# Kernel tuning notes

Hardware: AMD Instinct MI355X
Metric: run time of the kernel (lower is better)

The kernel has to match this reference:

```python
import jax, jax.numpy as jnp
import numpy as np


def quantize_uniform(x, n_bits, clip):
    # clamp to [-clip, clip], round to 2^(1-n_bits)*clip grid, cap at clip*(1-b)
    b = 2.0 ** (1 - n_bits)
    xc = jnp.clip(x, -clip, clip)
    return clip * jnp.minimum(b * jnp.round(xc / (b * clip)), 1.0 - b)


def quantize_act(x, n_bits, clip):
    # clip to [0, clip], round to 2^-n_bits grid, cap at 1 - 2^-n_bits
    s = 2.0 ** n_bits
    xc = jnp.clip(x, 0.0, clip)
    return jnp.minimum(jnp.round(xc * s) / s, 1.0 - 1.0 / s)


def qconv(x, w, b, pad):
    # fake-quantized conv: weights/bias quant(8,1), input quant(8,4), output quant(8,8)
    wq = quantize_uniform(w, 8, 1.0)
    bq = quantize_uniform(b, 8, 1.0)
    xq = quantize_uniform(x, 8, 4.0)
    y = jax.lax.conv_general_dilated(
        xq, wq, window_strides=(1, 1), padding=[(pad, pad), (pad, pad)],
        dimension_numbers=('NCHW', 'OIHW', 'NCHW'))
    y = y + bq[None, :, None, None]
    return quantize_uniform(y, 8, 8.0)


def setup_inputs() -> dict:
    key = jax.random.key(0)
    ks = jax.random.split(key, 7)
    N, Cin, H, W = 32, 128, 56, 56
    Sq, E1, E3 = 32, 128, 128
    x = jax.random.normal(ks[0], (N, Cin, H, W), dtype=jnp.float32)
    w_sq = jax.random.normal(ks[1], (Sq, Cin, 1, 1), dtype=jnp.float32) * 0.05
    b_sq = jax.random.normal(ks[2], (Sq,), dtype=jnp.float32) * 0.05
    w_e1 = jax.random.normal(ks[3], (E1, Sq, 1, 1), dtype=jnp.float32) * 0.05
    b_e1 = jax.random.normal(ks[4], (E1,), dtype=jnp.float32) * 0.05
    w_e3 = jax.random.normal(ks[5], (E3, Sq, 3, 3), dtype=jnp.float32) * 0.05
    b_e3 = jax.random.normal(ks[6], (E3,), dtype=jnp.float32) * 0.05
    return {'x': x, 'w_sq': w_sq, 'b_sq': b_sq, 'w_e1': w_e1, 'b_e1': b_e1,
            'w_e3': w_e3, 'b_e3': b_e3}


def reference(x, w_sq, b_sq, w_e1, b_e1, w_e3, b_e3):
    h = jax.nn.relu(qconv(x, w_sq, b_sq, pad=0))
    h = quantize_act(h, 13, 4.0)
    y1 = jax.nn.relu(qconv(h, w_e1, b_e1, pad=0))
    y3 = jax.nn.relu(qconv(h, w_e3, b_e3, pad=1))
    return jnp.concatenate([y1, y3], axis=1)
```

## Files before the change

### kernel.cpp

```cpp
#include <hip/hip_runtime.h>
#include <stdint.h>

typedef __bf16 bf16x8 __attribute__((ext_vector_type(8)));
typedef float  f32x4  __attribute__((ext_vector_type(4)));

#define HW   3136
#define WID  56
#define CIN  128
#define SQ   32

#define OFF_BSQ 0
#define OFF_BE  32
#define WSQF_BYTES_OFF 1152
#define WE1F_BYTES_OFF 9344
#define WE3F_BYTES_OFF 17536

__device__ __forceinline__ float quant_w8(float x){
  float xc = fminf(fmaxf(x,-1.f),1.f);
  return fminf(rintf(xc*128.f)*0.0078125f, 0.9921875f);
}
__device__ __forceinline__ ushort wq_int_bf16(float x){
  float xc = fminf(fmaxf(x,-1.f),1.f);
  float n = fminf(rintf(xc*128.f), 127.f);
  return (ushort)(__float_as_uint(n)>>16);
}
__device__ __forceinline__ uint pack2f(float a, float b){
  return (__float_as_uint(a)>>16) | (__float_as_uint(b)&0xffff0000u);
}

__global__ void prep_kernel(const float* __restrict__ wsq, const float* __restrict__ bsq,
                            const float* __restrict__ we1, const float* __restrict__ be1,
                            const float* __restrict__ we3, const float* __restrict__ be3,
                            float* __restrict__ ws){
  int tid = blockIdx.x*blockDim.x+threadIdx.x;
  int nth = gridDim.x*blockDim.x;
  ushort* wsqf = (ushort*)((char*)ws + WSQF_BYTES_OFF);
  ushort* we1f = (ushort*)((char*)ws + WE1F_BYTES_OFF);
  ushort* we3f = (ushort*)((char*)ws + WE3F_BYTES_OFF);
  for (int i=tid;i<SQ;i+=nth) ws[OFF_BSQ+i]=quant_w8(bsq[i]);
  for (int i=tid;i<256;i+=nth) ws[OFF_BE+i] = (i<128)? quant_w8(be1[i]) : quant_w8(be3[i-128]);
  for (int i=tid;i<4096;i+=nth){
    int mfkc=i>>9, l=(i>>3)&63, j=i&7;
    int mf=mfkc>>2, kc=mfkc&3;
    int co=mf*16+(l&15), ci=kc*32+(l>>4)*8+j;
    wsqf[i] = wq_int_bf16(wsq[co*CIN+ci]);
  }
  for (int i=tid;i<4096;i+=nth){
    int mf=i>>9, l=(i>>3)&63, j=i&7;
    int co=mf*16+(l&15), ci=(l>>4)*8+j;
    we1f[i] = wq_int_bf16(we1[co*SQ+ci]);
  }
  for (int i=tid;i<36864;i+=nth){
    int mf=i/4608, r=i-mf*4608, t=r>>9, l=(r>>3)&63, j=r&7;
    int co=mf*16+(l&15), ci=(l>>4)*8+j;
    we3f[i] = wq_int_bf16(we3[(co*SQ+ci)*9+t]);
  }
}

__global__ __launch_bounds__(512, 2) void fire_kernel(const float* __restrict__ x,
    const float* __restrict__ ws, float* __restrict__ out){
  __shared__ uint4 lds4[2320];
  int wg = blockIdx.x;
  int logical = (wg & 7)*28 + (wg >> 3);
  int n   = logical/7;
  int bry = logical - n*7;
  int tid = threadIdx.x, w = tid>>6, lane = tid&63;
  int colg = lane&15, kg = lane>>4;
  int R0 = bry*8;
  int vr0 = (R0==0) ? 0 : R0-1;
  int vr1 = (R0+8 > 55) ? 55 : R0+8;
  int limit = (vr1+1)*WID;
  int nblk = ((vr1-vr0+1)*WID + 15)>>4;
  int base_px = vr0*WID;

  uint4 z = make_uint4(0,0,0,0);
  for (int i=tid; i<2320; i+=512) lds4[i] = z;
  __syncthreads();

  {
    const bf16x8* wsqf = (const bf16x8*)((const char*)ws + WSQF_BYTES_OFF);
    bf16x8 W[8];
    #pragma unroll
    for (int q=0;q<8;++q) W[q] = wsqf[q*64 + lane];
    float bias[2][4];
    #pragma unroll
    for (int mf=0;mf<2;++mf)
      #pragma unroll
      for (int r=0;r<4;++r) bias[mf][r] = ws[OFF_BSQ + mf*16 + kg*4 + r];

    for (int b=w; b<nblk; b+=8){
      int px = base_px + b*16 + colg;
      int pxc = (px < limit) ? px : (limit-1);
      const float* xp = x + (size_t)n*CIN*HW + pxc;
      float xv[32];
      #pragma unroll
      for (int kc=0;kc<4;++kc)
        #pragma unroll
        for (int j=0;j<8;++j)
          xv[kc*8+j] = xp[(size_t)(kc*32 + kg*8 + j)*HW];

      bf16x8 Bf[4];
      #pragma unroll
      for (int kc=0;kc<4;++kc){
        float m[8];
        #pragma unroll
        for (int j=0;j<8;++j){
          float v = fminf(fmaxf(xv[kc*8+j],-4.f),4.f);
          m[j] = fminf(rintf(v*32.f), 127.f);
        }
        union { uint u[4]; bf16x8 v; } cv;
        #pragma unroll
        for (int q=0;q<4;++q) cv.u[q] = pack2f(m[q*2], m[q*2+1]);
        Bf[kc] = cv.v;
      }

      f32x4 acc0 = (f32x4){0.f,0.f,0.f,0.f};
      f32x4 acc1 = (f32x4){0.f,0.f,0.f,0.f};
      #pragma unroll
      for (int kc=0;kc<4;++kc){
        acc0 = __builtin_amdgcn_mfma_f32_16x16x32_bf16(W[kc],   Bf[kc], acc0, 0,0,0);
        acc1 = __builtin_amdgcn_mfma_f32_16x16x32_bf16(W[4+kc], Bf[kc], acc1, 0,0,0);
      }

      if (px < limit){
        int rr = px/WID, c = px - rr*WID;
        int ph = (rr - R0 + 1)*58 + c + 1;
        #pragma unroll
        for (int mf=0;mf<2;++mf){
          f32x4 a = mf ? acc1 : acc0;
          float m[4];
          #pragma unroll
          for (int r=0;r<4;++r){
            float y = fmaf(a[r], 0.000244140625f, bias[mf][r]);
            y = fminf(fmaxf(y,-8.f),8.f);
            y = fminf(rintf(y*16.f)*0.0625f, 7.9375f);
            y = fmaxf(y,0.f);
            y = fminf(y,4.f);
            y = fminf(y,0.9998779296875f);
            m[r] = rintf(y*32.f);
          }
          int chunk = mf*2 + (kg>>1);
          int idx = ph*4 + (chunk ^ ((ph>>1)&3));
          uint* dst = (uint*)&lds4[idx] + (kg&1)*2;
          dst[0] = pack2f(m[0], m[1]);
          dst[1] = pack2f(m[2], m[3]);
        }
      }
    }
  }
  __syncthreads();

  int wid = w&3, rpl = w>>2;
  const bf16x8* we1f = (const bf16x8*)((const char*)ws + WE1F_BYTES_OFF);
  const bf16x8* we3f = (const bf16x8*)((const char*)ws + WE3F_BYTES_OFF);
  const bf16x8* lbase = (const bf16x8*)lds4;

  #pragma unroll
  for (int s=0; s<2; ++s){
    int rp = rpl*2 + s;
    int baseh[7];
    #pragma unroll
    for (int nf=0;nf<7;++nf){
      int p = rp*112 + nf*16 + colg;
      int rr = p/WID, c = p - rr*WID;
      baseh[nf] = (rr+1)*58 + c + 1;
    }

    f32x4 acc[4][7];
    #pragma unroll
    for (int mi=0;mi<4;++mi)
      #pragma unroll
      for (int nf=0;nf<7;++nf)
        acc[mi][nf] = (f32x4){0.f,0.f,0.f,0.f};

    #pragma unroll
    for (int t=0;t<9;++t){
      int off = (t/3 - 1)*58 + (t%3 - 1);
      bf16x8 B[7];
      #pragma unroll
      for (int nf=0;nf<7;++nf){
        int ph = baseh[nf] + off;
        int idx = ph*4 + (kg ^ ((ph>>1)&3));
        B[nf] = lbase[idx];
      }
      bf16x8 A2 = we3f[(wid*9+t)*64 + lane];
      bf16x8 A3 = we3f[((wid+4)*9+t)*64 + lane];
      #pragma unroll
      for (int nf=0;nf<7;++nf){
        acc[2][nf] = __builtin_amdgcn_mfma_f32_16x16x32_bf16(B[nf], A2, acc[2][nf], 0,0,0);
        acc[3][nf] = __builtin_amdgcn_mfma_f32_16x16x32_bf16(B[nf], A3, acc[3][nf], 0,0,0);
      }
      if (t==4){
        bf16x8 A0 = we1f[wid*64 + lane];
        bf16x8 A1 = we1f[(wid+4)*64 + lane];
        #pragma unroll
        for (int nf=0;nf<7;++nf){
          acc[0][nf] = __builtin_amdgcn_mfma_f32_16x16x32_bf16(B[nf], A0, acc[0][nf], 0,0,0);
          acc[1][nf] = __builtin_amdgcn_mfma_f32_16x16x32_bf16(B[nf], A1, acc[1][nf], 0,0,0);
        }
      }
    }

    #pragma unroll
    for (int mi=0;mi<4;++mi){
      int co = (wid+mi*4)*16 + colg;
      float bias = ws[OFF_BE + co];
      float* opb = out + (size_t)(n*256+co)*HW + R0*WID + rp*112 + kg*4;
      #pragma unroll
      for (int nf=0;nf<7;++nf){
        f32x4 a = acc[mi][nf];
        f32x4 yv;
        #pragma unroll
        for (int r=0;r<4;++r){
          float y = fmaf(a[r], 0.000244140625f, bias);
          y = fminf(fmaxf(y,-8.f),8.f);
          y = fminf(rintf(y*16.f)*0.0625f, 7.9375f);
          y = fmaxf(y,0.f);
          yv[r] = y;
        }
        *(f32x4*)(opb + nf*16) = yv;
      }
    }
  }
}

extern "C" void kernel_launch(void* const* d_in, const int* in_sizes, int n_in,
                              void* d_out, int out_size, void* d_ws, size_t ws_size,
                              hipStream_t stream){
  const float* x   = (const float*)d_in[0];
  const float* wsq = (const float*)d_in[1];
  const float* bsq = (const float*)d_in[2];
  const float* we1 = (const float*)d_in[3];
  const float* be1 = (const float*)d_in[4];
  const float* we3 = (const float*)d_in[5];
  const float* be3 = (const float*)d_in[6];
  float* out = (float*)d_out;
  float* ws  = (float*)d_ws;

  hipLaunchKernelGGL(prep_kernel, dim3(64), dim3(256), 0, stream,
                     wsq, bsq, we1, be1, we3, be3, ws);
  hipLaunchKernelGGL(fire_kernel, dim3(224), dim3(512), 0, stream, x, ws, out);
}
```

Measured before the change: 43.40 us.

## Fuse weight prep into main kernel and stage quantized weights in LDS

Drops the separate prep kernel launch. Each workgroup now quantizes the squeeze, expand1x1 and expand3x3 weights itself, writes them into shared memory in MFMA fragment layout, and reads the expand weights from LDS instead of global memory. Biases are quantized inline. This removes a launch and the dependency between kernels. In exchange every block repeats the weight quantization with strided global reads, and the extra ~88KB of LDS probably limits occupancy to one block per CU. The epilogue is rewritten with a different channel mapping and leaves a dead loop behind.

Result: slower. 52.72 us (+21.5%).

```diff
diff --git a/kernel.cpp b/kernel.cpp
--- a/kernel.cpp
+++ b/kernel.cpp
@@ -9,57 +9,28 @@
 #define CIN  128
 #define SQ   32
 
-#define OFF_BSQ 0
-#define OFF_BE  32
-#define WSQF_BYTES_OFF 1152
-#define WE1F_BYTES_OFF 9344
-#define WE3F_BYTES_OFF 17536
-
 __device__ __forceinline__ float quant_w8(float x){
   float xc = fminf(fmaxf(x,-1.f),1.f);
   return fminf(rintf(xc*128.f)*0.0078125f, 0.9921875f);
 }
-__device__ __forceinline__ ushort wq_int_bf16(float x){
+__device__ __forceinline__ float wq_int_f(float x){
   float xc = fminf(fmaxf(x,-1.f),1.f);
-  float n = fminf(rintf(xc*128.f), 127.f);
-  return (ushort)(__float_as_uint(n)>>16);
+  return fminf(rintf(xc*128.f), 127.f);
 }
 __device__ __forceinline__ uint pack2f(float a, float b){
   return (__float_as_uint(a)>>16) | (__float_as_uint(b)&0xffff0000u);
 }
 
-__global__ void prep_kernel(const float* __restrict__ wsq, const float* __restrict__ bsq,
-                            const float* __restrict__ we1, const float* __restrict__ be1,
-                            const float* __restrict__ we3, const float* __restrict__ be3,
-                            float* __restrict__ ws){
-  int tid = blockIdx.x*blockDim.x+threadIdx.x;
-  int nth = gridDim.x*blockDim.x;
-  ushort* wsqf = (ushort*)((char*)ws + WSQF_BYTES_OFF);
-  ushort* we1f = (ushort*)((char*)ws + WE1F_BYTES_OFF);
-  ushort* we3f = (ushort*)((char*)ws + WE3F_BYTES_OFF);
-  for (int i=tid;i<SQ;i+=nth) ws[OFF_BSQ+i]=quant_w8(bsq[i]);
-  for (int i=tid;i<256;i+=nth) ws[OFF_BE+i] = (i<128)? quant_w8(be1[i]) : quant_w8(be3[i-128]);
-  for (int i=tid;i<4096;i+=nth){
-    int mfkc=i>>9, l=(i>>3)&63, j=i&7;
-    int mf=mfkc>>2, kc=mfkc&3;
-    int co=mf*16+(l&15), ci=kc*32+(l>>4)*8+j;
-    wsqf[i] = wq_int_bf16(wsq[co*CIN+ci]);
-  }
-  for (int i=tid;i<4096;i+=nth){
-    int mf=i>>9, l=(i>>3)&63, j=i&7;
-    int co=mf*16+(l&15), ci=(l>>4)*8+j;
-    we1f[i] = wq_int_bf16(we1[co*SQ+ci]);
-  }
-  for (int i=tid;i<36864;i+=nth){
-    int mf=i/4608, r=i-mf*4608, t=r>>9, l=(r>>3)&63, j=r&7;
-    int co=mf*16+(l&15), ci=(l>>4)*8+j;
-    we3f[i] = wq_int_bf16(we3[(co*SQ+ci)*9+t]);
-  }
-}
-
-__global__ __launch_bounds__(512, 2) void fire_kernel(const float* __restrict__ x,
-    const float* __restrict__ ws, float* __restrict__ out){
+__global__ __launch_bounds__(512) void fire_kernel(const float* __restrict__ x,
+    const float* __restrict__ wsq, const float* __restrict__ bsq,
+    const float* __restrict__ we1, const float* __restrict__ be1,
+    const float* __restrict__ we3, const float* __restrict__ be3,
+    float* __restrict__ out){
   __shared__ uint4 lds4[2320];
+  __shared__ ushort wsqf_l[4096];
+  __shared__ ushort we1f_l[4096];
+  __shared__ ushort we3f_l[36864];
+
   int wg = blockIdx.x;
   int logical = (wg & 7)*28 + (wg >> 3);
   int n   = logical/7;
@@ -73,20 +44,55 @@
   int nblk = ((vr1-vr0+1)*WID + 15)>>4;
   int base_px = vr0*WID;
 
-  uint4 z = make_uint4(0,0,0,0);
-  for (int i=tid; i<2320; i+=512) lds4[i] = z;
+  {
+    uint4 z = make_uint4(0,0,0,0);
+    for (int i=tid; i<2320; i+=512) lds4[i] = z;
+    {
+      int i = tid*8;
+      int mfkc=i>>9, l=(i>>3)&63;
+      int mf=mfkc>>2, kc=mfkc&3;
+      int co=mf*16+(l&15), cib=kc*32+(l>>4)*8;
+      const float* src = wsq + co*CIN + cib;
+      uint pk[4];
+      #pragma unroll
+      for (int q=0;q<4;++q)
+        pk[q] = pack2f(wq_int_f(src[q*2]), wq_int_f(src[q*2+1]));
+      *(uint4*)&wsqf_l[i] = make_uint4(pk[0],pk[1],pk[2],pk[3]);
+    }
+    {
+      int i = tid*8;
+      int mf=i>>9, l=(i>>3)&63;
+      int co=mf*16+(l&15), cib=(l>>4)*8;
+      const float* src = we1 + co*SQ + cib;
+      uint pk[4];
+      #pragma unroll
+      for (int q=0;q<4;++q)
+        pk[q] = pack2f(wq_int_f(src[q*2]), wq_int_f(src[q*2+1]));
+      *(uint4*)&we1f_l[i] = make_uint4(pk[0],pk[1],pk[2],pk[3]);
+    }
+    for (int g=tid; g<4608; g+=512){
+      int i = g*8;
+      int mf=i/4608, r=i-mf*4608, t=r>>9, l=(r>>3)&63;
+      int co=mf*16+(l&15), cib=(l>>4)*8;
+      const float* src = we3 + (size_t)(co*SQ+cib)*9 + t;
+      uint pk[4];
+      #pragma unroll
+      for (int q=0;q<4;++q)
+        pk[q] = pack2f(wq_int_f(src[(q*2)*9]), wq_int_f(src[(q*2+1)*9]));
+      *(uint4*)&we3f_l[i] = make_uint4(pk[0],pk[1],pk[2],pk[3]);
+    }
+  }
   __syncthreads();
 
   {
-    const bf16x8* wsqf = (const bf16x8*)((const char*)ws + WSQF_BYTES_OFF);
     bf16x8 W[8];
     #pragma unroll
-    for (int q=0;q<8;++q) W[q] = wsqf[q*64 + lane];
+    for (int q=0;q<8;++q) W[q] = *(const bf16x8*)&wsqf_l[(q*64 + lane)*8];
     float bias[2][4];
     #pragma unroll
     for (int mf=0;mf<2;++mf)
       #pragma unroll
-      for (int r=0;r<4;++r) bias[mf][r] = ws[OFF_BSQ + mf*16 + kg*4 + r];
+      for (int r=0;r<4;++r) bias[mf][r] = quant_w8(bsq[mf*16 + kg*4 + r]);
 
     for (int b=w; b<nblk; b+=8){
       int px = base_px + b*16 + colg;
@@ -151,8 +157,6 @@
   __syncthreads();
 
   int wid = w&3, rpl = w>>2;
-  const bf16x8* we1f = (const bf16x8*)((const char*)ws + WE1F_BYTES_OFF);
-  const bf16x8* we3f = (const bf16x8*)((const char*)ws + WE3F_BYTES_OFF);
   const bf16x8* lbase = (const bf16x8*)lds4;
 
   #pragma unroll
@@ -183,16 +187,16 @@
         int idx = ph*4 + (kg ^ ((ph>>1)&3));
         B[nf] = lbase[idx];
       }
-      bf16x8 A2 = we3f[(wid*9+t)*64 + lane];
-      bf16x8 A3 = we3f[((wid+4)*9+t)*64 + lane];
+      bf16x8 A2 = *(const bf16x8*)&we3f_l[((wid*9+t)*64 + lane)*8];
+      bf16x8 A3 = *(const bf16x8*)&we3f_l[(((wid+4)*9+t)*64 + lane)*8];
       #pragma unroll
       for (int nf=0;nf<7;++nf){
         acc[2][nf] = __builtin_amdgcn_mfma_f32_16x16x32_bf16(B[nf], A2, acc[2][nf], 0,0,0);
         acc[3][nf] = __builtin_amdgcn_mfma_f32_16x16x32_bf16(B[nf], A3, acc[3][nf], 0,0,0);
       }
       if (t==4){
-        bf16x8 A0 = we1f[wid*64 + lane];
-        bf16x8 A1 = we1f[(wid+4)*64 + lane];
+        bf16x8 A0 = *(const bf16x8*)&we1f_l[(wid*64 + lane)*8];
+        bf16x8 A1 = *(const bf16x8*)&we1f_l[((wid+4)*64 + lane)*8];
         #pragma unroll
         for (int nf=0;nf<7;++nf){
           acc[0][nf] = __builtin_amdgcn_mfma_f32_16x16x32_bf16(B[nf], A0, acc[0][nf], 0,0,0);
@@ -204,11 +208,28 @@
     #pragma unroll
     for (int mi=0;mi<4;++mi){
       int co = (wid+mi*4)*16 + colg;
-      float bias = ws[OFF_BE + co];
-      float* opb = out + (size_t)(n*256+co)*HW + R0*WID + rp*112 + kg*4;
+      float bias_e1 = quant_w8(be1[co]);
+      float bias_e3 = quant_w8(be3[co]);
+      float* op1 = out + (size_t)(n*256+co)*HW + R0*WID + rp*112 + kg*4;
+      float* op3 = out + (size_t)(n*256+128+co)*HW + R0*WID + rp*112 + kg*4;
       #pragma unroll
       for (int nf=0;nf<7;++nf){
         f32x4 a = acc[mi][nf];
+        (void)a;
+      }
+      (void)op1; (void)op3; (void)bias_e1; (void)bias_e3;
+    }
+    #pragma unroll
+    for (int mi=0;mi<4;++mi){
+      int g = (mi&1) ? (wid+4) : wid;
+      int co = g*16 + colg;
+      bool is_e3 = (mi>=2);
+      int src = is_e3 ? (2 + (mi&1)) : (mi&1);
+      float bias = is_e3 ? quant_w8(be3[co]) : quant_w8(be1[co]);
+      float* opb = out + (size_t)(n*256 + (is_e3?128:0) + co)*HW + R0*WID + rp*112 + kg*4;
+      #pragma unroll
+      for (int nf=0;nf<7;++nf){
+        f32x4 a = acc[src][nf];
         f32x4 yv;
         #pragma unroll
         for (int r=0;r<4;++r){
@@ -235,9 +256,7 @@
   const float* we3 = (const float*)d_in[5];
   const float* be3 = (const float*)d_in[6];
   float* out = (float*)d_out;
-  float* ws  = (float*)d_ws;
-
-  hipLaunchKernelGGL(prep_kernel, dim3(64), dim3(256), 0, stream,
-                     wsq, bsq, we1, be1, we3, be3, ws);
-  hipLaunchKernelGGL(fire_kernel, dim3(224), dim3(512), 0, stream, x, ws, out);
-}
+
+  hipLaunchKernelGGL(fire_kernel, dim3(224), dim3(512), 0, stream,
+                     x, wsq, bsq, we1, be1, we3, be3, out);
+}
```
